# Optimization experiments

Measured on AMD Instinct MI355X. Metric: run time of the kernel, lower is better.

## Reference

```python
import jax, jax.numpy as jnp
import numpy as np

E = 1024
H = 16
D = E // H  # head_dim = 64
B, S = 8, 1024


def setup_inputs() -> dict:
    key = jax.random.key(0)
    ks = jax.random.split(key, 5)
    x = jax.random.normal(ks[0], (B, S, E), dtype=jnp.float32)
    # nn.Linear(E, 3E): weight [3E, E], bias [3E]
    w_in = jax.random.normal(ks[1], (3 * E, E), dtype=jnp.float32) * (1.0 / np.sqrt(E))
    b_in = jax.random.normal(ks[2], (3 * E,), dtype=jnp.float32) * 0.02
    # nn.Linear(E, E)
    w_out = jax.random.normal(ks[3], (E, E), dtype=jnp.float32) * (1.0 / np.sqrt(E))
    b_out = jax.random.normal(ks[4], (E,), dtype=jnp.float32) * 0.02
    return {"x": x, "w_in": w_in, "b_in": b_in, "w_out": w_out, "b_out": b_out}


def reference(x, w_in, b_in, w_out, b_out):
    Bb, Ss, _ = x.shape
    # fused QKV projection: x @ W.T + b -> [B, S, 3E]
    qkv = jnp.einsum('bse,fe->bsf', x, w_in) + b_in
    # reshape to [B, H, S, 3D] then split
    qkv = qkv.reshape(Bb, Ss, H, 3 * D).transpose(0, 2, 1, 3)
    q, k, v = jnp.split(qkv, 3, axis=-1)  # each [B, H, S, D]
    scale = 1.0 / jnp.sqrt(jnp.asarray(D, dtype=x.dtype))
    logits = jnp.einsum('bhqd,bhkd->bhqk', q, k) * scale  # [B, H, S, S]
    attn = jax.nn.softmax(logits, axis=-1)
    values = jnp.einsum('bhqk,bhkd->bhqd', attn, v)  # [B, H, S, D]
    values = values.transpose(0, 2, 1, 3).reshape(Bb, Ss, E)
    out = jnp.einsum('bse,fe->bsf', values, w_out) + b_out
    return out
```

## Files before the change

kernel.cpp:

```cpp
#include <hip/hip_runtime.h>

typedef short short8 __attribute__((ext_vector_type(8)));
typedef float f32x4 __attribute__((ext_vector_type(4)));

#define AS1 __attribute__((address_space(1)))
#define AS3 __attribute__((address_space(3)))

__device__ __forceinline__ void gload16(const void* g, void* l) {
    __builtin_amdgcn_global_load_lds((const AS1 unsigned int*)g, (AS3 unsigned int*)l, 16, 0, 0);
}

__device__ __forceinline__ unsigned short f2bf(float f) {
    union { float f; unsigned u; } c; c.f = f;
    unsigned r = (c.u + 0x7FFFu + ((c.u >> 16) & 1u)) >> 16;
    return (unsigned short)r;
}

__device__ __forceinline__ unsigned cvtpk(float a, float b) {
    unsigned r;
    asm("v_cvt_pk_bf16_f32 %0, %1, %2" : "=v"(r) : "v"(a), "v"(b));
    return r;
}

__device__ __forceinline__ void mfma16(f32x4& d, short8 a, short8 b) {
    asm("v_mfma_f32_16x16x32_bf16 %0, %1, %2, %0" : "+v"(d) : "v"(a), "v"(b));
}

#define QSCALE 0.18033688011112042f

__global__ __launch_bounds__(256) void cvt_f32_bf16(const float* __restrict__ in,
                                                    unsigned short* __restrict__ out, int n4) {
    int idx = blockIdx.x * 256 + threadIdx.x;
    int stride = gridDim.x * 256;
    for (int i = idx; i < n4; i += stride) {
        float4 v = ((const float4*)in)[i];
        ushort4 o;
        o.x = f2bf(v.x); o.y = f2bf(v.y); o.z = f2bf(v.z); o.w = f2bf(v.w);
        ((ushort4*)out)[i] = o;
    }
}

template <int EPI>
__global__ __launch_bounds__(256) void gemm_nt(
    const unsigned short* __restrict__ A, const unsigned short* __restrict__ B,
    const float* __restrict__ bias, int M, int N, int K,
    float* __restrict__ Cf, unsigned short* __restrict__ qb,
    unsigned short* __restrict__ kb, unsigned short* __restrict__ vtb) {
    __shared__ unsigned short As[128 * 64];
    __shared__ unsigned short Bs[128 * 64];
    const int tid = threadIdx.x;
    const int lane = tid & 63;
    const int wv = tid >> 6;
    const int wm = (wv >> 1) * 64, wn = (wv & 1) * 64;
    const int lr = lane & 15, lg = lane >> 4;
    const int x7 = lr & 7;
    const int m0 = blockIdx.x * 128, n0 = blockIdx.y * 128;

    f32x4 acc[4][4];
#pragma unroll
    for (int i = 0; i < 4; i++)
#pragma unroll
        for (int j = 0; j < 4; j++) acc[i][j] = (f32x4){0.f, 0.f, 0.f, 0.f};

    const int sr = tid >> 3;
    const int sc = ((tid & 7) ^ ((tid >> 3) & 7)) * 8;
    const unsigned short* Ag = A + (size_t)(m0 + sr) * K + sc;
    const unsigned short* Bg = B + (size_t)(n0 + sr) * K + sc;
    unsigned short* Asl = As + tid * 8;
    unsigned short* Bsl = Bs + tid * 8;

    for (int kt = 0; kt < K; kt += 64) {
        __syncthreads();
#pragma unroll
        for (int i = 0; i < 4; i++) {
            gload16(Ag + (size_t)(i * 32) * K + kt, Asl + i * 2048);
            gload16(Bg + (size_t)(i * 32) * K + kt, Bsl + i * 2048);
        }
        __syncthreads();
#pragma unroll
        for (int ks = 0; ks < 2; ks++) {
            short8 af[4], bf[4];
#pragma unroll
            for (int mi = 0; mi < 4; mi++)
                af[mi] = *(const short8*)(As + (wm + mi * 16 + lr) * 64 +
                                          (((ks * 4 + lg) ^ x7) * 8));
#pragma unroll
            for (int ni = 0; ni < 4; ni++)
                bf[ni] = *(const short8*)(Bs + (wn + ni * 16 + lr) * 64 +
                                          (((ks * 4 + lg) ^ x7) * 8));
#pragma unroll
            for (int mi = 0; mi < 4; mi++)
#pragma unroll
                for (int ni = 0; ni < 4; ni++) mfma16(acc[mi][ni], af[mi], bf[ni]);
        }
    }

#pragma unroll
    for (int ni = 0; ni < 4; ni++) {
        const int col = n0 + wn + ni * 16 + lr;
        const float bia = bias[col];
        const unsigned h = (unsigned)col / 192u;
        const int rem = col - (int)h * 192;
        const int tq = rem >> 6, d = rem & 63;
#pragma unroll
        for (int mi = 0; mi < 4; mi++) {
            const int row = m0 + wm + mi * 16 + lg * 4;
            if (EPI == 1) {
#pragma unroll
                for (int r = 0; r < 4; r++)
                    Cf[(size_t)(row + r) * N + col] = acc[mi][ni][r] + bia;
            } else {
                const int bb = row >> 10, s = row & 1023;
                const int bh = bb * 16 + (int)h;
                if (tq == 0) {
#pragma unroll
                    for (int r = 0; r < 4; r++)
                        qb[((size_t)bh * 1024 + s + r) * 64 + d] =
                            f2bf((acc[mi][ni][r] + bia) * QSCALE);
                } else if (tq == 1) {
#pragma unroll
                    for (int r = 0; r < 4; r++)
                        kb[((size_t)bh * 1024 + s + r) * 64 + d] = f2bf(acc[mi][ni][r] + bia);
                } else {
                    uint2 pk;
                    pk.x = cvtpk(acc[mi][ni][0] + bia, acc[mi][ni][1] + bia);
                    pk.y = cvtpk(acc[mi][ni][2] + bia, acc[mi][ni][3] + bia);
                    *(uint2*)(vtb + ((size_t)bh * 64 + d) * 1024 + s) = pk;
                }
            }
        }
    }
}

__device__ __forceinline__ void softmax_half(f32x4 (&s)[4], float& m, float& l,
                                             f32x4 (&o)[4], unsigned short* pbuf,
                                             int lr, int lg, int x7) {
    float mx = s[0][0];
#pragma unroll
    for (int kt = 0; kt < 4; kt++)
#pragma unroll
        for (int r = 0; r < 4; r++) mx = fmaxf(mx, s[kt][r]);
    mx = fmaxf(mx, __shfl_xor(mx, 16));
    mx = fmaxf(mx, __shfl_xor(mx, 32));
    const float mn = fmaxf(m, mx);
    const float alpha = __builtin_amdgcn_exp2f(m - mn);
    m = mn;
    float p[4][4];
    float rs = 0.f;
#pragma unroll
    for (int kt = 0; kt < 4; kt++)
#pragma unroll
        for (int r = 0; r < 4; r++) {
            p[kt][r] = __builtin_amdgcn_exp2f(s[kt][r] - mn);
            rs += p[kt][r];
        }
    rs += __shfl_xor(rs, 16);
    rs += __shfl_xor(rs, 32);
    l = l * alpha + rs;
#pragma unroll
    for (int mi = 0; mi < 4; mi++)
#pragma unroll
        for (int r = 0; r < 4; r++) o[mi][r] *= alpha;
#pragma unroll
    for (int kt = 0; kt < 4; kt++)
#pragma unroll
        for (int w2 = 0; w2 < 2; w2++) {
            const unsigned pk = cvtpk(p[kt][2 * w2], p[kt][2 * w2 + 1]);
            const int col = (kt * 16 + lg * 4 + 2 * w2) ^ (x7 << 3);
            *(unsigned*)(pbuf + lr * 64 + col) = pk;
        }
}

__global__ __launch_bounds__(256) void attn_fwd(
    const unsigned short* __restrict__ qg, const unsigned short* __restrict__ kg,
    const unsigned short* __restrict__ vtg, unsigned short* __restrict__ vals) {
    __shared__ unsigned short Ks[64 * 64];
    __shared__ unsigned short Vts[64 * 64];
    __shared__ unsigned short Ps[4 * 2048];
    const int tid = threadIdx.x, lane = tid & 63, w = tid >> 6;
    const int lr = lane & 15, lg = lane >> 4;
    const int x7 = lr & 7;
    const int bh = blockIdx.y;
    const int q0 = blockIdx.x * 128 + w * 32;

    const unsigned short* qrowA = qg + ((size_t)bh * 1024 + q0 + lr) * 64;
    const unsigned short* qrowB = qrowA + 16 * 64;
    short8 qA[2], qB[2];
    qA[0] = *(const short8*)(qrowA + lg * 8);
    qA[1] = *(const short8*)(qrowA + 32 + lg * 8);
    qB[0] = *(const short8*)(qrowB + lg * 8);
    qB[1] = *(const short8*)(qrowB + 32 + lg * 8);

    f32x4 oA[4], oB[4];
    float mA = -1e30f, mB = -1e30f, lA = 0.f, lB = 0.f;
#pragma unroll
    for (int i = 0; i < 4; i++) {
        oA[i] = (f32x4){0.f, 0.f, 0.f, 0.f};
        oB[i] = (f32x4){0.f, 0.f, 0.f, 0.f};
    }

    const unsigned short* kb = kg + (size_t)bh * 65536;
    const unsigned short* vb = vtg + (size_t)bh * 65536;
    unsigned short* pwl = Ps + w * 2048;

    const int srow = tid >> 3;
    const int scol = ((tid & 7) ^ (srow & 7)) * 8;

    for (int kv0 = 0; kv0 < 1024; kv0 += 64) {
        __syncthreads();
#pragma unroll
        for (int i = 0; i < 2; i++) {
            gload16(kb + (size_t)(kv0 + i * 32 + srow) * 64 + scol, Ks + i * 2048 + tid * 8);
            gload16(vb + (size_t)(i * 32 + srow) * 1024 + kv0 + scol, Vts + i * 2048 + tid * 8);
        }
        __syncthreads();

        f32x4 sA[4], sB[4];
#pragma unroll
        for (int i = 0; i < 4; i++) {
            sA[i] = (f32x4){0.f, 0.f, 0.f, 0.f};
            sB[i] = (f32x4){0.f, 0.f, 0.f, 0.f};
        }
#pragma unroll
        for (int kt = 0; kt < 4; kt++) {
            const short8 k0 = *(const short8*)(Ks + (kt * 16 + lr) * 64 + ((0 + lg) ^ x7) * 8);
            const short8 k1 = *(const short8*)(Ks + (kt * 16 + lr) * 64 + ((4 + lg) ^ x7) * 8);
            mfma16(sA[kt], k0, qA[0]);
            mfma16(sB[kt], k0, qB[0]);
            mfma16(sA[kt], k1, qA[1]);
            mfma16(sB[kt], k1, qB[1]);
        }

        softmax_half(sA, mA, lA, oA, pwl, lr, lg, x7);
        softmax_half(sB, mB, lB, oB, pwl + 1024, lr, lg, x7);

        short8 pA[2], pB[2];
#pragma unroll
        for (int ks2 = 0; ks2 < 2; ks2++) {
            pA[ks2] = *(const short8*)(pwl + lr * 64 + (((ks2 * 4 + lg) ^ x7) * 8));
            pB[ks2] = *(const short8*)(pwl + 1024 + lr * 64 + (((ks2 * 4 + lg) ^ x7) * 8));
        }
#pragma unroll
        for (int mi = 0; mi < 4; mi++) {
            const short8 v0 = *(const short8*)(Vts + (mi * 16 + lr) * 64 + ((0 + lg) ^ x7) * 8);
            const short8 v1 = *(const short8*)(Vts + (mi * 16 + lr) * 64 + ((4 + lg) ^ x7) * 8);
            mfma16(oA[mi], v0, pA[0]);
            mfma16(oB[mi], v0, pB[0]);
            mfma16(oA[mi], v1, pA[1]);
            mfma16(oB[mi], v1, pB[1]);
        }
    }

    const int bb = bh >> 4, hh = bh & 15;
    {
        const float inv = 1.f / lA;
        unsigned short* vp = vals + (size_t)(bb * 1024 + q0 + lr) * 1024 + hh * 64 + lg * 4;
#pragma unroll
        for (int mi = 0; mi < 4; mi++) {
            uint2 st;
            st.x = cvtpk(oA[mi][0] * inv, oA[mi][1] * inv);
            st.y = cvtpk(oA[mi][2] * inv, oA[mi][3] * inv);
            *(uint2*)(vp + mi * 16) = st;
        }
    }
    {
        const float inv = 1.f / lB;
        unsigned short* vp = vals + (size_t)(bb * 1024 + q0 + 16 + lr) * 1024 + hh * 64 + lg * 4;
#pragma unroll
        for (int mi = 0; mi < 4; mi++) {
            uint2 st;
            st.x = cvtpk(oB[mi][0] * inv, oB[mi][1] * inv);
            st.y = cvtpk(oB[mi][2] * inv, oB[mi][3] * inv);
            *(uint2*)(vp + mi * 16) = st;
        }
    }
}

extern "C" void kernel_launch(void* const* d_in, const int* in_sizes, int n_in,
                              void* d_out, int out_size, void* d_ws, size_t ws_size,
                              hipStream_t stream) {
    const float* x = (const float*)d_in[0];
    const float* w_in = (const float*)d_in[1];
    const float* b_in = (const float*)d_in[2];
    const float* w_out = (const float*)d_in[3];
    const float* b_out = (const float*)d_in[4];
    float* out = (float*)d_out;

    unsigned short* ws = (unsigned short*)d_ws;
    unsigned short* xb = ws;
    unsigned short* winb = xb + 8388608;
    unsigned short* woutb = winb + 3145728;
    unsigned short* qb = woutb + 1048576;
    unsigned short* kb = qb + 8388608;
    unsigned short* vtb = kb + 8388608;
    unsigned short* vals = xb;

    cvt_f32_bf16<<<2048, 256, 0, stream>>>(x, xb, 8388608 / 4);
    cvt_f32_bf16<<<1024, 256, 0, stream>>>(w_in, winb, 3145728 / 4);
    cvt_f32_bf16<<<512, 256, 0, stream>>>(w_out, woutb, 1048576 / 4);

    gemm_nt<0><<<dim3(64, 24), 256, 0, stream>>>(xb, winb, b_in, 8192, 3072, 1024,
                                                 nullptr, qb, kb, vtb);
    attn_fwd<<<dim3(8, 128), 256, 0, stream>>>(qb, kb, vtb, vals);
    gemm_nt<1><<<dim3(64, 8), 256, 0, stream>>>(vals, woutb, b_out, 8192, 1024, 1024,
                                                out, nullptr, nullptr, nullptr);
}
```

Measured before the change: 161.6 us.

## Fuse conversion kernels, raise MFMA wave priority, reorder attention grid

Merges the three fp32-to-bf16 conversion launches into a single grid-stride kernel that dispatches on index range, removing two launches and their tails. Wraps the MFMA blocks in the GEMM and attention kernels with s_setprio raise/lower so waves issuing matrix ops get scheduling priority over waves loading. Swaps the attention grid so blockIdx.x indexes batch-head and blockIdx.y indexes the query block, which changes dispatch order and the L2 locality of K/V. The fused conversion adds per-element branches, and the priority hints may have no effect or may reorder memory issue badly.

```diff
diff --git a/kernel.cpp b/kernel.cpp
--- a/kernel.cpp
+++ b/kernel.cpp
@@ -28,15 +28,32 @@
 
 #define QSCALE 0.18033688011112042f
 
-__global__ __launch_bounds__(256) void cvt_f32_bf16(const float* __restrict__ in,
-                                                    unsigned short* __restrict__ out, int n4) {
+#define XN4 2097152
+#define WIN4 786432
+#define WOUT4 262144
+__global__ __launch_bounds__(256) void cvt_all(const float* __restrict__ x,
+                                               const float* __restrict__ w_in,
+                                               const float* __restrict__ w_out,
+                                               unsigned short* __restrict__ xb,
+                                               unsigned short* __restrict__ winb,
+                                               unsigned short* __restrict__ woutb) {
     int idx = blockIdx.x * 256 + threadIdx.x;
     int stride = gridDim.x * 256;
-    for (int i = idx; i < n4; i += stride) {
-        float4 v = ((const float4*)in)[i];
+    for (int i = idx; i < XN4 + WIN4 + WOUT4; i += stride) {
+        const float4* src;
+        ushort4* dst;
+        int j;
+        if (i < XN4) {
+            src = (const float4*)x; dst = (ushort4*)xb; j = i;
+        } else if (i < XN4 + WIN4) {
+            src = (const float4*)w_in; dst = (ushort4*)winb; j = i - XN4;
+        } else {
+            src = (const float4*)w_out; dst = (ushort4*)woutb; j = i - XN4 - WIN4;
+        }
+        float4 v = src[j];
         ushort4 o;
         o.x = f2bf(v.x); o.y = f2bf(v.y); o.z = f2bf(v.z); o.w = f2bf(v.w);
-        ((ushort4*)out)[i] = o;
+        dst[j] = o;
     }
 }
 
@@ -88,10 +105,12 @@
             for (int ni = 0; ni < 4; ni++)
                 bf[ni] = *(const short8*)(Bs + (wn + ni * 16 + lr) * 64 +
                                           (((ks * 4 + lg) ^ x7) * 8));
+            __builtin_amdgcn_s_setprio(1);
 #pragma unroll
             for (int mi = 0; mi < 4; mi++)
 #pragma unroll
                 for (int ni = 0; ni < 4; ni++) mfma16(acc[mi][ni], af[mi], bf[ni]);
+            __builtin_amdgcn_s_setprio(0);
         }
     }
 
@@ -180,8 +199,8 @@
     const int tid = threadIdx.x, lane = tid & 63, w = tid >> 6;
     const int lr = lane & 15, lg = lane >> 4;
     const int x7 = lr & 7;
-    const int bh = blockIdx.y;
-    const int q0 = blockIdx.x * 128 + w * 32;
+    const int bh = blockIdx.x;
+    const int q0 = blockIdx.y * 128 + w * 32;
 
     const unsigned short* qrowA = qg + ((size_t)bh * 1024 + q0 + lr) * 64;
     const unsigned short* qrowB = qrowA + 16 * 64;
@@ -225,10 +244,12 @@
         for (int kt = 0; kt < 4; kt++) {
             const short8 k0 = *(const short8*)(Ks + (kt * 16 + lr) * 64 + ((0 + lg) ^ x7) * 8);
             const short8 k1 = *(const short8*)(Ks + (kt * 16 + lr) * 64 + ((4 + lg) ^ x7) * 8);
+            __builtin_amdgcn_s_setprio(1);
             mfma16(sA[kt], k0, qA[0]);
             mfma16(sB[kt], k0, qB[0]);
             mfma16(sA[kt], k1, qA[1]);
             mfma16(sB[kt], k1, qB[1]);
+            __builtin_amdgcn_s_setprio(0);
         }
 
         softmax_half(sA, mA, lA, oA, pwl, lr, lg, x7);
@@ -244,10 +265,12 @@
         for (int mi = 0; mi < 4; mi++) {
             const short8 v0 = *(const short8*)(Vts + (mi * 16 + lr) * 64 + ((0 + lg) ^ x7) * 8);
             const short8 v1 = *(const short8*)(Vts + (mi * 16 + lr) * 64 + ((4 + lg) ^ x7) * 8);
+            __builtin_amdgcn_s_setprio(1);
             mfma16(oA[mi], v0, pA[0]);
             mfma16(oB[mi], v0, pB[0]);
             mfma16(oA[mi], v1, pA[1]);
             mfma16(oB[mi], v1, pB[1]);
+            __builtin_amdgcn_s_setprio(0);
         }
     }
 
@@ -295,13 +318,11 @@
     unsigned short* vtb = kb + 8388608;
     unsigned short* vals = xb;
 
-    cvt_f32_bf16<<<2048, 256, 0, stream>>>(x, xb, 8388608 / 4);
-    cvt_f32_bf16<<<1024, 256, 0, stream>>>(w_in, winb, 3145728 / 4);
-    cvt_f32_bf16<<<512, 256, 0, stream>>>(w_out, woutb, 1048576 / 4);
+    cvt_all<<<2048, 256, 0, stream>>>(x, w_in, w_out, xb, winb, woutb);
 
     gemm_nt<0><<<dim3(64, 24), 256, 0, stream>>>(xb, winb, b_in, 8192, 3072, 1024,
                                                  nullptr, qb, kb, vtb);
-    attn_fwd<<<dim3(8, 128), 256, 0, stream>>>(qb, kb, vtb, vals);
+    attn_fwd<<<dim3(128, 8), 256, 0, stream>>>(qb, kb, vtb, vals);
     gemm_nt<1><<<dim3(64, 8), 256, 0, stream>>>(vals, woutb, b_out, 8192, 1024, 1024,
                                                 out, nullptr, nullptr, nullptr);
 }
```

Result: faster. 157.6 us (-2.5%).
